# Kernel optimization log

Measured on AMD Instinct MI355X. Metric: run time of the kernel, lower is better.

## Reference

```python
import jax, jax.numpy as jnp
import numpy as np

N_GRAPHS = 200
NODES_PER_GRAPH = 500
N_NODES = N_GRAPHS * NODES_PER_GRAPH
N_EDGES = 3_200_000
D = 256
H = 64  # = in_channels // 4, and predictor hidden_dim
RATIO_NORM = 600.0


def setup_inputs() -> dict:
    key = jax.random.key(0)
    ks = jax.random.split(key, 12)
    x = jax.random.normal(ks[0], (N_NODES, D), dtype=jnp.float32)
    # score MLP: Linear(D, D//4) -> ReLU -> Linear(D//4, 1)
    Ws1 = jax.random.normal(ks[1], (D, H), dtype=jnp.float32) * (1.0 / np.sqrt(D))
    bs1 = jnp.zeros((H,), jnp.float32)
    Ws2 = jax.random.normal(ks[2], (H, 1), dtype=jnp.float32) * (1.0 / np.sqrt(H))
    bs2 = jnp.zeros((1,), jnp.float32)
    # KeepRatioPredictor: Linear(3, 64) -> ReLU -> Linear(64, 1) -> Sigmoid
    Wp1 = jax.random.normal(ks[3], (3, H), dtype=jnp.float32) * 0.5
    bp1 = jnp.zeros((H,), jnp.float32)
    Wp2 = jax.random.normal(ks[4], (H, 1), dtype=jnp.float32) * (1.0 / np.sqrt(H))
    bp2 = jnp.zeros((1,), jnp.float32)
    # edges with both endpoints inside the same graph block (for density)
    blk = jax.random.randint(ks[5], (N_EDGES,), 0, N_GRAPHS, dtype=jnp.int32)
    src = blk * NODES_PER_GRAPH + jax.random.randint(ks[6], (N_EDGES,), 0, NODES_PER_GRAPH, dtype=jnp.int32)
    dst = blk * NODES_PER_GRAPH + jax.random.randint(ks[7], (N_EDGES,), 0, NODES_PER_GRAPH, dtype=jnp.int32)
    return {
        "x": x, "Ws1": Ws1, "bs1": bs1, "Ws2": Ws2, "bs2": bs2,
        "Wp1": Wp1, "bp1": bp1, "Wp2": Wp2, "bp2": bp2,
        "edges_src": src, "edges_dst": dst, "nodes_per_graph": NODES_PER_GRAPH,
    }


def reference(x, Ws1, bs1, Ws2, bs2, Wp1, bp1, Wp2, bp2,
              edges_src, edges_dst, nodes_per_graph):
    N, C = x.shape
    n = nodes_per_graph            # python int
    G = N // n
    # node scores (dropout in eval mode -> identity)
    score = (jax.nn.relu(x @ Ws1 + bs1) @ Ws2 + bs2)[:, 0]       # [N]
    s = score.reshape(G, n)                                        # [G, n]
    # per-graph density: count edges whose both endpoints lie in the graph
    eg_s = edges_src // n
    eg_d = edges_dst // n
    same = (eg_s == eg_d).astype(jnp.float32)
    counts = jax.ops.segment_sum(same, eg_s, num_segments=G)      # [G]
    density = counts / float(n * (n - 1))
    avg_score = s.mean(axis=1)                                     # [G]
    # batched KeepRatioPredictor
    feats = jnp.stack(
        [jnp.full((G,), n / RATIO_NORM, dtype=jnp.float32), avg_score, density],
        axis=1)                                                    # [G, 3]
    keep_ratio = jax.nn.sigmoid(jax.nn.relu(feats @ Wp1 + bp1) @ Wp2 + bp2)[:, 0]
    keep_num = jnp.maximum(2, (n * keep_ratio).astype(jnp.int32))  # [G]
    # per-graph top-k mask: rank within graph (descending) < keep_num
    order = jnp.argsort(-s, axis=1)
    ranks = jnp.argsort(order, axis=1)                             # [G, n]
    mask = (ranks < keep_num[:, None]).reshape(-1)                 # [N] bool
    # gated, padded pooled features: kept rows = x * tanh(score), others zero
    x_pooled = x * jnp.tanh(score)[:, None] * mask[:, None].astype(x.dtype)
    return (x_pooled, mask)
```

## Files before the change

kernel.cpp:

```cpp
#include <hip/hip_runtime.h>
#include <math.h>

#define NPG 500
#define DIM 256
#define HID 64
#define RATIO_NORM 600.0f

__global__ __launch_bounds__(256) void k_score(
    const float* __restrict__ x,
    const float* __restrict__ Ws1,
    const float* __restrict__ bs1,
    const float* __restrict__ Ws2,
    const float* __restrict__ bs2,
    float* __restrict__ score, int N)
{
    int node = blockIdx.x * 256 + threadIdx.x;
    int nodec = node < N ? node : (N - 1);
    const float4* xr = reinterpret_cast<const float4*>(x + (size_t)nodec * DIM);

    float acc[HID];
#pragma unroll
    for (int h = 0; h < HID; ++h) acc[h] = bs1[h];

    for (int k4 = 0; k4 < DIM / 4; ++k4) {
        float4 xv = xr[k4];
        const float* w = Ws1 + (size_t)(k4 * 4) * HID;
#pragma unroll
        for (int h = 0; h < HID; ++h) {
            acc[h] = fmaf(xv.x, w[h],           acc[h]);
            acc[h] = fmaf(xv.y, w[HID + h],     acc[h]);
            acc[h] = fmaf(xv.z, w[2 * HID + h], acc[h]);
            acc[h] = fmaf(xv.w, w[3 * HID + h], acc[h]);
        }
    }
    float sc = bs2[0];
#pragma unroll
    for (int h = 0; h < HID; ++h)
        sc = fmaf(fmaxf(acc[h], 0.0f), Ws2[h], sc);
    if (node < N) score[node] = sc;
}

__global__ __launch_bounds__(256) void k_edges(
    const int* __restrict__ esrc, const int* __restrict__ edst,
    int* __restrict__ counts, int E, int G)
{
    __shared__ int hist[256];
    for (int i = threadIdx.x; i < G; i += 256) hist[i] = 0;
    __syncthreads();

    int nchunk = E >> 2;
    const int4* s4 = reinterpret_cast<const int4*>(esrc);
    const int4* d4 = reinterpret_cast<const int4*>(edst);
    for (int c = blockIdx.x * 256 + threadIdx.x; c < nchunk; c += gridDim.x * 256) {
        int4 s = s4[c], d = d4[c];
        int g;
        g = s.x / NPG; if (g == d.x / NPG) atomicAdd(&hist[g], 1);
        g = s.y / NPG; if (g == d.y / NPG) atomicAdd(&hist[g], 1);
        g = s.z / NPG; if (g == d.z / NPG) atomicAdd(&hist[g], 1);
        g = s.w / NPG; if (g == d.w / NPG) atomicAdd(&hist[g], 1);
    }
    if (blockIdx.x == 0) {
        for (int e = (nchunk << 2) + threadIdx.x; e < E; e += 256) {
            int g = esrc[e] / NPG;
            if (g == edst[e] / NPG) atomicAdd(&hist[g], 1);
        }
    }
    __syncthreads();
    for (int i = threadIdx.x; i < G; i += 256)
        if (hist[i]) atomicAdd(&counts[i], hist[i]);
}

__global__ __launch_bounds__(256) void k_keep(
    const float* __restrict__ score,
    const int* __restrict__ counts,
    const float* __restrict__ Wp1,
    const float* __restrict__ bp1,
    const float* __restrict__ Wp2,
    const float* __restrict__ bp2,
    int* __restrict__ keep_num)
{
    int g = blockIdx.x;
    __shared__ float red[256];
    const float* s = score + (size_t)g * NPG;
    float v = 0.0f;
    for (int i = threadIdx.x; i < NPG; i += 256) v += s[i];
    red[threadIdx.x] = v;
    __syncthreads();
    for (int off = 128; off >= 1; off >>= 1) {
        if (threadIdx.x < off) red[threadIdx.x] += red[threadIdx.x + off];
        __syncthreads();
    }
    if (threadIdx.x < 64) {
        float f0 = (float)NPG / RATIO_NORM;
        float f1 = red[0] / (float)NPG;
        float f2 = (float)counts[g] / (float)(NPG * (NPG - 1));
        int h = threadIdx.x;
        float hv = bp1[h];
        hv = fmaf(f0, Wp1[h], hv);
        hv = fmaf(f1, Wp1[HID + h], hv);
        hv = fmaf(f2, Wp1[2 * HID + h], hv);
        hv = fmaxf(hv, 0.0f) * Wp2[h];
#pragma unroll
        for (int m = 32; m >= 1; m >>= 1) hv += __shfl_xor(hv, m, 64);
        if (h == 0) {
            float z = hv + bp2[0];
            float kr = 1.0f / (1.0f + expf(-z));
            int kn = (int)((float)NPG * kr);
            keep_num[g] = kn < 2 ? 2 : kn;
        }
    }
}

__global__ __launch_bounds__(256) void k_mask_out(
    const float* __restrict__ x,
    const float* __restrict__ score,
    const int* __restrict__ keep_num,
    float* __restrict__ out_x,
    float* __restrict__ out_mask)
{
    int g = blockIdx.x;
    __shared__ float s[NPG];
    __shared__ float gate[NPG];
    const float* sg = score + (size_t)g * NPG;
    for (int i = threadIdx.x; i < NPG; i += 256) s[i] = sg[i];
    __syncthreads();

    int kn = keep_num[g];
    for (int i = threadIdx.x; i < NPG; i += 256) {
        float si = s[i];
        int rank = 0;
        for (int j = 0; j < NPG; ++j) {
            float sj = s[j];
            rank += (sj > si) || ((sj == si) && (j < i));
        }
        bool keep = rank < kn;
        out_mask[(size_t)g * NPG + i] = keep ? 1.0f : 0.0f;
        gate[i] = keep ? tanhf(si) : 0.0f;
    }
    __syncthreads();

    int lane = threadIdx.x & 63;
    int wrow = threadIdx.x >> 6;
    for (int r = wrow; r < NPG; r += 4) {
        float gt = gate[r];
        size_t base = ((size_t)g * NPG + r) * DIM;
        float4* o = reinterpret_cast<float4*>(out_x + base);
        if (gt != 0.0f) {
            const float4* xi = reinterpret_cast<const float4*>(x + base);
            float4 v = xi[lane];
            o[lane] = make_float4(v.x * gt, v.y * gt, v.z * gt, v.w * gt);
        } else {
            o[lane] = make_float4(0.0f, 0.0f, 0.0f, 0.0f);
        }
    }
}

extern "C" void kernel_launch(void* const* d_in, const int* in_sizes, int n_in,
                              void* d_out, int out_size, void* d_ws, size_t ws_size,
                              hipStream_t stream)
{
    const float* x   = (const float*)d_in[0];
    const float* Ws1 = (const float*)d_in[1];
    const float* bs1 = (const float*)d_in[2];
    const float* Ws2 = (const float*)d_in[3];
    const float* bs2 = (const float*)d_in[4];
    const float* Wp1 = (const float*)d_in[5];
    const float* bp1 = (const float*)d_in[6];
    const float* Wp2 = (const float*)d_in[7];
    const float* bp2 = (const float*)d_in[8];
    const int* esrc  = (const int*)d_in[9];
    const int* edst  = (const int*)d_in[10];

    int E = in_sizes[9];
    int N = in_sizes[0] / DIM;
    int G = N / NPG;

    float* score  = (float*)d_ws;
    int* counts   = (int*)((char*)d_ws + (size_t)N * sizeof(float));
    int* keep     = counts + G;

    float* out_x    = (float*)d_out;
    float* out_mask = out_x + (size_t)N * DIM;

    hipMemsetAsync(counts, 0, G * sizeof(int), stream);
    k_score<<<(N + 255) / 256, 256, 0, stream>>>(x, Ws1, bs1, Ws2, bs2, score, N);
    k_edges<<<512, 256, 0, stream>>>(esrc, edst, counts, E, G);
    k_keep<<<G, 256, 0, stream>>>(score, counts, Wp1, bp1, Wp2, bp2, keep);
    k_mask_out<<<G, 256, 0, stream>>>(x, score, keep, out_x, out_mask);
}
```

Before: 162.9 us.

## Split score MLP across 8 lanes per node and decouple gated write kernel

The score kernel now assigns 8 threads per node, each computing 8 hidden units with vectorized weight loads, then reduces the partial dot products with warp shuffles. This cuts the per-thread register footprint from 64 accumulators and raises parallelism from 100k threads to 800k. The former mask/output kernel is split so ranking writes gates to workspace, and a separate row-parallel kernel does the large gated copy across many blocks instead of only 200. Each lane group now rereads the same x row, and there is an extra launch plus a gate round-trip through global memory.

```diff
diff --git a/kernel.cpp b/kernel.cpp
--- a/kernel.cpp
+++ b/kernel.cpp
@@ -5,6 +5,7 @@
 #define DIM 256
 #define HID 64
 #define RATIO_NORM 600.0f
+#define LPN 8
 
 __global__ __launch_bounds__(256) void k_score(
     const float* __restrict__ x,
@@ -14,30 +15,49 @@
     const float* __restrict__ bs2,
     float* __restrict__ score, int N)
 {
-    int node = blockIdx.x * 256 + threadIdx.x;
+    int t = blockIdx.x * 256 + threadIdx.x;
+    int node = t / LPN;
+    int p = t & (LPN - 1);
+    int h0 = p * (HID / LPN);
     int nodec = node < N ? node : (N - 1);
     const float4* xr = reinterpret_cast<const float4*>(x + (size_t)nodec * DIM);
 
-    float acc[HID];
-#pragma unroll
-    for (int h = 0; h < HID; ++h) acc[h] = bs1[h];
+    float4 a0 = *reinterpret_cast<const float4*>(bs1 + h0);
+    float4 a1 = *reinterpret_cast<const float4*>(bs1 + h0 + 4);
 
     for (int k4 = 0; k4 < DIM / 4; ++k4) {
         float4 xv = xr[k4];
-        const float* w = Ws1 + (size_t)(k4 * 4) * HID;
+        const float* wb = Ws1 + (size_t)(k4 * 4) * HID + h0;
 #pragma unroll
-        for (int h = 0; h < HID; ++h) {
-            acc[h] = fmaf(xv.x, w[h],           acc[h]);
-            acc[h] = fmaf(xv.y, w[HID + h],     acc[h]);
-            acc[h] = fmaf(xv.z, w[2 * HID + h], acc[h]);
-            acc[h] = fmaf(xv.w, w[3 * HID + h], acc[h]);
-        }
-    }
-    float sc = bs2[0];
-#pragma unroll
-    for (int h = 0; h < HID; ++h)
-        sc = fmaf(fmaxf(acc[h], 0.0f), Ws2[h], sc);
-    if (node < N) score[node] = sc;
+        for (int kk = 0; kk < 4; ++kk) {
+            float xk = kk == 0 ? xv.x : kk == 1 ? xv.y : kk == 2 ? xv.z : xv.w;
+            float4 wa = *reinterpret_cast<const float4*>(wb + kk * HID);
+            float4 wc = *reinterpret_cast<const float4*>(wb + kk * HID + 4);
+            a0.x = fmaf(xk, wa.x, a0.x);
+            a0.y = fmaf(xk, wa.y, a0.y);
+            a0.z = fmaf(xk, wa.z, a0.z);
+            a0.w = fmaf(xk, wa.w, a0.w);
+            a1.x = fmaf(xk, wc.x, a1.x);
+            a1.y = fmaf(xk, wc.y, a1.y);
+            a1.z = fmaf(xk, wc.z, a1.z);
+            a1.w = fmaf(xk, wc.w, a1.w);
+        }
+    }
+    float4 w0 = *reinterpret_cast<const float4*>(Ws2 + h0);
+    float4 w1 = *reinterpret_cast<const float4*>(Ws2 + h0 + 4);
+    float sc = 0.0f;
+    sc = fmaf(fmaxf(a0.x, 0.0f), w0.x, sc);
+    sc = fmaf(fmaxf(a0.y, 0.0f), w0.y, sc);
+    sc = fmaf(fmaxf(a0.z, 0.0f), w0.z, sc);
+    sc = fmaf(fmaxf(a0.w, 0.0f), w0.w, sc);
+    sc = fmaf(fmaxf(a1.x, 0.0f), w1.x, sc);
+    sc = fmaf(fmaxf(a1.y, 0.0f), w1.y, sc);
+    sc = fmaf(fmaxf(a1.z, 0.0f), w1.z, sc);
+    sc = fmaf(fmaxf(a1.w, 0.0f), w1.w, sc);
+    sc += __shfl_xor(sc, 1, 64);
+    sc += __shfl_xor(sc, 2, 64);
+    sc += __shfl_xor(sc, 4, 64);
+    if (p == 0 && node < N) score[node] = sc + bs2[0];
 }
 
 __global__ __launch_bounds__(256) void k_edges(
@@ -111,16 +131,14 @@
     }
 }
 
-__global__ __launch_bounds__(256) void k_mask_out(
-    const float* __restrict__ x,
+__global__ __launch_bounds__(256) void k_rank(
     const float* __restrict__ score,
     const int* __restrict__ keep_num,
-    float* __restrict__ out_x,
-    float* __restrict__ out_mask)
+    float* __restrict__ out_mask,
+    float* __restrict__ gate)
 {
     int g = blockIdx.x;
     __shared__ float s[NPG];
-    __shared__ float gate[NPG];
     const float* sg = score + (size_t)g * NPG;
     for (int i = threadIdx.x; i < NPG; i += 256) s[i] = sg[i];
     __syncthreads();
@@ -134,24 +152,29 @@
             rank += (sj > si) || ((sj == si) && (j < i));
         }
         bool keep = rank < kn;
-        out_mask[(size_t)g * NPG + i] = keep ? 1.0f : 0.0f;
-        gate[i] = keep ? tanhf(si) : 0.0f;
-    }
-    __syncthreads();
-
+        size_t idx = (size_t)g * NPG + i;
+        out_mask[idx] = keep ? 1.0f : 0.0f;
+        gate[idx] = keep ? tanhf(si) : 0.0f;
+    }
+}
+
+__global__ __launch_bounds__(256) void k_write(
+    const float* __restrict__ x,
+    const float* __restrict__ gate,
+    float* __restrict__ out_x, int N)
+{
     int lane = threadIdx.x & 63;
-    int wrow = threadIdx.x >> 6;
-    for (int r = wrow; r < NPG; r += 4) {
-        float gt = gate[r];
-        size_t base = ((size_t)g * NPG + r) * DIM;
-        float4* o = reinterpret_cast<float4*>(out_x + base);
-        if (gt != 0.0f) {
-            const float4* xi = reinterpret_cast<const float4*>(x + base);
-            float4 v = xi[lane];
-            o[lane] = make_float4(v.x * gt, v.y * gt, v.z * gt, v.w * gt);
-        } else {
-            o[lane] = make_float4(0.0f, 0.0f, 0.0f, 0.0f);
-        }
+    int row = blockIdx.x * 4 + (threadIdx.x >> 6);
+    if (row >= N) return;
+    float gt = gate[row];
+    size_t base = (size_t)row * DIM;
+    float4* o = reinterpret_cast<float4*>(out_x + base);
+    if (gt != 0.0f) {
+        const float4* xi = reinterpret_cast<const float4*>(x + base);
+        float4 v = xi[lane];
+        o[lane] = make_float4(v.x * gt, v.y * gt, v.z * gt, v.w * gt);
+    } else {
+        o[lane] = make_float4(0.0f, 0.0f, 0.0f, 0.0f);
     }
 }
 
@@ -175,16 +198,18 @@
     int N = in_sizes[0] / DIM;
     int G = N / NPG;
 
-    float* score  = (float*)d_ws;
-    int* counts   = (int*)((char*)d_ws + (size_t)N * sizeof(float));
-    int* keep     = counts + G;
+    float* score = (float*)d_ws;
+    float* gate  = score + N;
+    int* counts  = (int*)(gate + N);
+    int* keep    = counts + G;
 
     float* out_x    = (float*)d_out;
     float* out_mask = out_x + (size_t)N * DIM;
 
     hipMemsetAsync(counts, 0, G * sizeof(int), stream);
-    k_score<<<(N + 255) / 256, 256, 0, stream>>>(x, Ws1, bs1, Ws2, bs2, score, N);
+    k_score<<<(N * LPN + 255) / 256, 256, 0, stream>>>(x, Ws1, bs1, Ws2, bs2, score, N);
     k_edges<<<512, 256, 0, stream>>>(esrc, edst, counts, E, G);
     k_keep<<<G, 256, 0, stream>>>(score, counts, Wp1, bp1, Wp2, bp2, keep);
-    k_mask_out<<<G, 256, 0, stream>>>(x, score, keep, out_x, out_mask);
-}
+    k_rank<<<G, 256, 0, stream>>>(score, keep, out_mask, gate);
+    k_write<<<(N + 3) / 4, 256, 0, stream>>>(x, gate, out_x, N);
+}
```

After: 282.8 us. +73.6%, slower.
